# Kernel tuning notes

Measured on AMD Instinct MI355X. Metric: run time of the kernel, lower is better.

Reference implementation:

```python
import jax, jax.numpy as jnp
import numpy as np

# ---- static config (mirrors Spectral2xDown.__init__) ----
B, C_IN, C_OUT = 2, 256, 256
H_HI, W_HI = 256, 512
H_LO, W_LO = 128, 256
LMAX = H_LO            # 128
MMAX = W_LO // 2 + 1   # 129
GROUPS = 32
EPS_GN = 1e-5


def _cc_nodes_weights(n):
    """Clenshaw-Curtis nodes x_j=cos(pi*j/(n-1)) and quadrature weights on [-1,1]
    (torch_harmonics 'equiangular' grid)."""
    N = n - 1
    tj = np.pi * np.arange(n) / N
    xj = np.cos(tj)
    ks = np.arange(1, N // 2 + 1)
    b = np.where(2 * ks == N, 1.0, 2.0)
    s = (b / (4.0 * ks**2 - 1.0))[None, :] * np.cos(2.0 * ks[None, :] * tj[:, None])
    w = (2.0 / N) * (1.0 - s.sum(axis=1))
    w[0] = w[-1] = (1.0 / N**2) if (N % 2) else (1.0 / (N**2 - 1.0))
    return xj, w


def _legpoly(mmax, lmax, x):
    """Orthonormal associated Legendre (-1)^m c_lm P_lm(x), shape [mmax,lmax,len(x)]
    (torch_harmonics _precompute_legpoly, norm='ortho', csphase=True)."""
    nmax = max(mmax, lmax)
    vdm = np.zeros((nmax, nmax, len(x)))
    vdm[0, 0] = 1.0 / np.sqrt(4.0 * np.pi)
    for l in range(1, nmax):
        vdm[l - 1, l] = np.sqrt(2 * l + 1) * x * vdm[l - 1, l - 1]
        vdm[l, l] = np.sqrt((2 * l + 1) * (1 + x) * (1 - x) / (2 * l)) * vdm[l - 1, l - 1]
    for l in range(2, nmax):
        for m in range(0, l - 1):
            vdm[m, l] = (x * np.sqrt((2 * l - 1) / (l - m) * (2 * l + 1) / (l + m)) * vdm[m, l - 1]
                         - np.sqrt((l + m - 1) / (l - m) * (2 * l + 1) / (2 * l - 3)
                                   * (l - m - 1) / (l + m)) * vdm[m, l - 2])
    vdm = vdm[:mmax, :lmax].copy()
    for m in range(1, mmax, 2):  # Condon-Shortley phase
        vdm[m] *= -1.0
    return vdm


def _precompute():
    ct_hi, w_hi = _cc_nodes_weights(H_HI)
    pct_hi = _legpoly(MMAX, LMAX, np.flip(np.arccos(ct_hi)) * 0 + np.cos(np.flip(np.arccos(ct_hi))))
    wmat_hi = pct_hi * w_hi[None, None, :]          # quadrature folded in: [M,L,K_hi]
    ct_lo, _ = _cc_nodes_weights(H_LO)
    pct_lo = _legpoly(MMAX, LMAX, np.cos(np.flip(np.arccos(ct_lo))))  # [M,L,K_lo]
    return wmat_hi.astype(np.float32), pct_lo.astype(np.float32)


def setup_inputs() -> dict:
    key = jax.random.key(0)
    k1, k2 = jax.random.split(key, 2)
    x = jax.random.normal(k1, (B, C_IN, H_HI, W_HI), jnp.float32)
    conv_w = jax.random.normal(k2, (C_OUT, C_IN), jnp.float32) / np.sqrt(C_IN)
    conv_b = jnp.zeros((C_OUT,), jnp.float32)
    gamma = jnp.ones((C_OUT,), jnp.float32)
    beta = jnp.zeros((C_OUT,), jnp.float32)
    wmat_hi, pct_lo = _precompute()
    return {"x": x, "conv_w": conv_w, "conv_b": conv_b, "gamma": gamma, "beta": beta,
            "wmat_hi": jnp.asarray(wmat_hi), "pct_lo": jnp.asarray(pct_lo)}


def reference(x, conv_w, conv_b, gamma, beta, wmat_hi, pct_lo):
    # --- forward real SHT on high-res grid (2*pi * rfft(norm='forward') + Legendre quadrature) ---
    X = (2.0 * jnp.pi / W_HI) * jnp.fft.rfft(x, axis=-1)     # [B,C,K_hi,W_HI//2+1]
    X = X[..., :MMAX]                                        # truncate to mmax
    flm_r = jnp.einsum('bckm,mlk->bclm', X.real, wmat_hi)    # [B,C,L,M]
    flm_i = jnp.einsum('bckm,mlk->bclm', X.imag, wmat_hi)
    # --- inverse real SHT on low-res grid ---
    g = (jnp.einsum('bclm,mlk->bckm', flm_r, pct_lo)
         + 1j * jnp.einsum('bclm,mlk->bckm', flm_i, pct_lo))  # [B,C,K_lo,M]
    y = jnp.fft.irfft(g, n=W_LO, axis=-1) * W_LO             # irfft norm='forward'
    # --- 1x1 conv -> GroupNorm(32) -> exact GELU ---
    h = jnp.einsum('bchw,oc->bohw', y, conv_w) + conv_b[None, :, None, None]
    hg = h.reshape(B, GROUPS, C_OUT // GROUPS, H_LO, W_LO)
    mu = hg.mean(axis=(2, 3, 4), keepdims=True)
    var = ((hg - mu) ** 2).mean(axis=(2, 3, 4), keepdims=True)
    hn = ((hg - mu) * jax.lax.rsqrt(var + EPS_GN)).reshape(B, C_OUT, H_LO, W_LO)
    out = hn * gamma[None, :, None, None] + beta[None, :, None, None]
    return jax.nn.gelu(out, approximate=False)
```

## Files before the change

### kernel.cpp

```cpp
#include <hip/hip_runtime.h>
#include <math.h>


#define ROWS_HI 131072
#define ROWS_LO 65536

#define B_FT    0LL
#define B_FIT   262144LL
#define B_WM    393216LL
#define B_PCT   8781824LL
#define B_WB    12976128LL
#define B_STATS 13107200LL
#define B_R1    13107712LL
#define B_R2    80216576LL

typedef __attribute__((ext_vector_type(8))) short bf16x8;
typedef __attribute__((ext_vector_type(8))) unsigned short ushort8;
typedef __attribute__((ext_vector_type(4))) unsigned short ushort4v;
typedef __attribute__((ext_vector_type(4))) float f32x4;

__device__ inline unsigned short f2bf(float f){
  unsigned int u = __float_as_uint(f);
  unsigned int r = u + 0x7FFFu + ((u >> 16) & 1u);
  return (unsigned short)(r >> 16);
}

__global__ __launch_bounds__(256) void k_tables(unsigned char* __restrict__ ws){
  unsigned short* FT  = (unsigned short*)(ws + B_FT);
  unsigned short* FIT = (unsigned short*)(ws + B_FIT);
  float* stats = (float*)(ws + B_STATS);
  int idx = blockIdx.x*256 + threadIdx.x;
  if (idx < 131072){
    int p = idx >> 9, w = idx & 511, m = p >> 1;
    int pr = (m*w) & 511;
    float ang = (float)pr * (float)(2.0*M_PI/512.0);
    float s, c; sincosf(ang, &s, &c);
    const float S = (float)(2.0*M_PI/512.0);
    FT[idx] = f2bf((p & 1) ? (-S*s) : (S*c));
  }
  int i2 = idx - 131072;
  if (i2 >= 0 && i2 < 65536){
    int w = i2 >> 8, p = i2 & 255, m = p >> 1;
    float eps = (m == 0) ? 1.f : 2.f;
    int pr = (m*w) & 255;
    float ang = (float)pr * (float)(2.0*M_PI/256.0);
    float s, c; sincosf(ang, &s, &c);
    FIT[i2] = f2bf((p & 1) ? (-eps*s) : (eps*c));
  }
  int i3 = idx - (131072 + 65536);
  if (i3 >= 0 && i3 < 128) stats[i3] = 0.f;
}

__global__ __launch_bounds__(256) void k_prep(const float* __restrict__ wmat,
                                              const float* __restrict__ pct,
                                              const float* __restrict__ Wc,
                                              unsigned char* __restrict__ ws){
  unsigned short* WM = (unsigned short*)(ws + B_WM);
  unsigned short* PT = (unsigned short*)(ws + B_PCT);
  unsigned short* WB = (unsigned short*)(ws + B_WB);
  int idx = blockIdx.x*256 + threadIdx.x;
  if (idx < 4194304){
    WM[idx] = f2bf(wmat[idx]);
  } else if (idx < 6291456){
    int j = idx - 4194304;
    int m = j >> 14, kp = (j >> 7) & 127, l = j & 127;
    PT[j] = f2bf(pct[m*16384 + l*128 + kp]);
  } else if (idx < 6356992){
    int j = idx - 6291456;
    WB[j] = f2bf(Wc[j]);
  }
}

template<int AMODE, int CMODE, bool BIAS, int MT, int NT, int SKIP, int WPE>
__global__ __launch_bounds__(256, WPE) void k_gemm(
    const float* __restrict__ Af,
    const unsigned short* __restrict__ Abf,
    const unsigned short* __restrict__ Bt,
    float* __restrict__ Cf,
    unsigned short* __restrict__ Cbf,
    const float* __restrict__ bias,
    int ldA, int ldB, int ldC, int ksteps,
    long long sA, long long sB, int bzsh, long long sC)
{
  constexpr int BM = MT*32;
  constexpr int BN = NT*32;
  __shared__ unsigned short As[BM][40];
  __shared__ unsigned short Bs[BN][40];
  const int tid = threadIdx.x;
  const int z = blockIdx.z;
  const int m = z >> 1;
  const long long offA = (long long)z * sA;
  const long long offB = (long long)(z >> bzsh) * sB;
  const long long offC = (long long)z * sC;
  const int row0 = blockIdx.x * BM;
  const int n0   = blockIdx.y * BN;
  const int lane = tid & 63;
  const int wv = tid >> 6;
  const int wm = wv >> 1, wn = wv & 1;
  const int fr = lane & 15, q = lane >> 4;

  f32x4 acc[MT][NT];
#pragma unroll
  for (int i=0;i<MT;++i)
#pragma unroll
    for (int j=0;j<NT;++j) acc[i][j] = (f32x4){0.f,0.f,0.f,0.f};

  int ks0 = (SKIP == 2) ? (m >> 5) : 0;
  for (int ks = ks0; ks < ksteps; ++ks){
    const int k0 = ks * 32;
    if (AMODE == 0){
      if (BM == 128){
        const int row = tid >> 1, half = tid & 1;
        const float* s = Af + offA + (long long)(row0 + row) * ldA + k0 + half*16;
        float vv[16];
        *(float4*)(vv+0)  = *(const float4*)(s+0);
        *(float4*)(vv+4)  = *(const float4*)(s+4);
        *(float4*)(vv+8)  = *(const float4*)(s+8);
        *(float4*)(vv+12) = *(const float4*)(s+12);
        ushort8 H0, H1;
#pragma unroll
        for (int j=0;j<8;++j){ H0[j] = f2bf(vv[j]); H1[j] = f2bf(vv[8+j]); }
        *(ushort8*)&As[row][half*16]   = H0;
        *(ushort8*)&As[row][half*16+8] = H1;
      } else {
        const int row = tid >> 2, qt = tid & 3;
        const float* s = Af + offA + (long long)(row0 + row) * ldA + k0 + qt*8;
        float vv[8];
        *(float4*)(vv+0) = *(const float4*)(s+0);
        *(float4*)(vv+4) = *(const float4*)(s+4);
        ushort8 H;
#pragma unroll
        for (int j=0;j<8;++j) H[j] = f2bf(vv[j]);
        *(ushort8*)&As[row][qt*8] = H;
      }
    } else if (BM == 256){
      const unsigned short* s = Abf + offA + (long long)(row0 + tid) * ldA + k0;
      *(ushort8*)&As[tid][0]  = *(const ushort8*)(s);
      *(ushort8*)&As[tid][8]  = *(const ushort8*)(s+8);
      *(ushort8*)&As[tid][16] = *(const ushort8*)(s+16);
      *(ushort8*)&As[tid][24] = *(const ushort8*)(s+24);
    } else if (BM == 128){
      const int row = tid >> 1, half = tid & 1;
      const unsigned short* s = Abf + offA + (long long)(row0 + row) * ldA + k0 + half*16;
      *(ushort8*)&As[row][half*16]   = *(const ushort8*)(s);
      *(ushort8*)&As[row][half*16+8] = *(const ushort8*)(s+8);
    } else {
      const int row = tid >> 2, qt = tid & 3;
      const unsigned short* s = Abf + offA + (long long)(row0 + row) * ldA + k0 + qt*8;
      *(ushort8*)&As[row][qt*8] = *(const ushort8*)(s);
    }
    if (BN == 256){
      const unsigned short* s = Bt + offB + (long long)(n0 + tid) * ldB + k0;
      *(ushort8*)&Bs[tid][0]  = *(const ushort8*)(s);
      *(ushort8*)&Bs[tid][8]  = *(const ushort8*)(s+8);
      *(ushort8*)&Bs[tid][16] = *(const ushort8*)(s+16);
      *(ushort8*)&Bs[tid][24] = *(const ushort8*)(s+24);
    } else if (BN == 128){
      const int row = tid >> 1, half = tid & 1;
      const unsigned short* s = Bt + offB + (long long)(n0 + row) * ldB + k0 + half*16;
      *(ushort8*)&Bs[row][half*16]   = *(const ushort8*)(s);
      *(ushort8*)&Bs[row][half*16+8] = *(const ushort8*)(s+8);
    } else {
      const int row = tid >> 2, qt = tid & 3;
      const unsigned short* s = Bt + offB + (long long)(n0 + row) * ldB + k0 + qt*8;
      *(ushort8*)&Bs[row][qt*8] = *(const ushort8*)(s);
    }
    __syncthreads();
    bf16x8 ah[MT];
#pragma unroll
    for (int mt=0;mt<MT;++mt)
      ah[mt] = *(const bf16x8*)&As[wm*(MT*16)+mt*16+fr][q*8];
#pragma unroll
    for (int nt=0;nt<NT;++nt){
      if (SKIP == 1 && (wn*(NT*16) + nt*16 + 16 <= m)) continue;
      bf16x8 bb = *(const bf16x8*)&Bs[wn*(NT*16)+nt*16+fr][q*8];
#pragma unroll
      for (int mt=0;mt<MT;++mt)
        acc[mt][nt] = __builtin_amdgcn_mfma_f32_16x16x32_bf16(ah[mt], bb, acc[mt][nt], 0,0,0);
    }
    __syncthreads();
  }

  if (CMODE == 0){
#pragma unroll
    for (int mt=0;mt<MT;++mt){
      int row = row0 + wm*(MT*16) + mt*16 + q*4;
      float bv0=0.f,bv1=0.f,bv2=0.f,bv3=0.f;
      if (BIAS){ bv0=bias[row]; bv1=bias[row+1]; bv2=bias[row+2]; bv3=bias[row+3]; }
#pragma unroll
      for (int nt=0;nt<NT;++nt){
        int col = n0 + wn*(NT*16) + nt*16 + fr;
        float* dst = Cf + offC + (long long)row * ldC + col;
        dst[0]                = acc[mt][nt][0] + bv0;
        dst[(long long)ldC]   = acc[mt][nt][1] + bv1;
        dst[(long long)ldC*2] = acc[mt][nt][2] + bv2;
        dst[(long long)ldC*3] = acc[mt][nt][3] + bv3;
      }
    }
  } else if (CMODE == 1){
#pragma unroll
    for (int nt=0;nt<NT;++nt){
      int colp = n0 + wn*(NT*16) + nt*16 + fr;
#pragma unroll
      for (int mt=0;mt<MT;++mt){
        int rowb = row0 + wm*(MT*16) + mt*16 + q*4;
        ushort4v h;
        h[0] = f2bf(acc[mt][nt][0]);
        h[1] = f2bf(acc[mt][nt][1]);
        h[2] = f2bf(acc[mt][nt][2]);
        h[3] = f2bf(acc[mt][nt][3]);
        *(ushort4v*)&Cbf[offC + (long long)colp * ldC + rowb] = h;
      }
    }
  } else {
#pragma unroll
    for (int mt=0;mt<MT;++mt){
      int row = row0 + wm*(MT*16) + mt*16 + q*4;
#pragma unroll
      for (int nt=0;nt<NT;++nt){
        int col = n0 + wn*(NT*16) + nt*16 + fr;
        unsigned short* dst = Cbf + offC + (long long)row * ldC + col;
        dst[0]      = f2bf(acc[mt][nt][0]);
        dst[ldC]    = f2bf(acc[mt][nt][1]);
        dst[ldC*2]  = f2bf(acc[mt][nt][2]);
        dst[ldC*3]  = f2bf(acc[mt][nt][3]);
      }
    }
  }
}

__global__ __launch_bounds__(256) void k_trb(const unsigned short* __restrict__ g,
                                             unsigned short* __restrict__ gT){
  __shared__ unsigned short t[64][68];
  const int r0 = blockIdx.x * 64;
  const int p0 = blockIdx.y * 64;
  const int tr = threadIdx.x & 15, tc = threadIdx.x >> 4;
#pragma unroll
  for (int i=0;i<4;++i){
    int pl = tc + i*16;
    ushort4v v = *(const ushort4v*)(g + (long long)(p0+pl)*ROWS_LO + r0 + tr*4);
    *(ushort4v*)&t[pl][tr*4] = v;
  }
  __syncthreads();
#pragma unroll
  for (int i=0;i<4;++i){
    int rl = tc + i*16;
    ushort4v w;
    w[0]=t[tr*4+0][rl]; w[1]=t[tr*4+1][rl]; w[2]=t[tr*4+2][rl]; w[3]=t[tr*4+3][rl];
    *(ushort4v*)(gT + (long long)(r0+rl)*256 + p0 + tr*4) = w;
  }
}

__global__ __launch_bounds__(256) void k_tr2(const float* __restrict__ y,
                                             unsigned short* __restrict__ yT){
  __shared__ float t[64][65];
  const int s0 = blockIdx.x * 64;
  const int c0 = blockIdx.y * 64;
  const int b  = blockIdx.z;
  const int tr = threadIdx.x & 15, tc = threadIdx.x >> 4;
#pragma unroll
  for (int i=0;i<4;++i){
    int cl = tc + i*16;
    float4 v = *(const float4*)(y + (long long)b*8388608 + (long long)(c0+cl)*32768 + s0 + tr*4);
    t[cl][tr*4+0]=v.x; t[cl][tr*4+1]=v.y; t[cl][tr*4+2]=v.z; t[cl][tr*4+3]=v.w;
  }
  __syncthreads();
#pragma unroll
  for (int i=0;i<4;++i){
    int sl = tc + i*16;
    ushort4v w;
    w[0]=f2bf(t[tr*4+0][sl]); w[1]=f2bf(t[tr*4+1][sl]);
    w[2]=f2bf(t[tr*4+2][sl]); w[3]=f2bf(t[tr*4+3][sl]);
    *(ushort4v*)(yT + (long long)b*8388608 + (long long)(s0+sl)*256 + c0 + tr*4) = w;
  }
}

__global__ __launch_bounds__(256) void k_stats(const float* __restrict__ h,
                                               float* __restrict__ stats){
  const int bg = blockIdx.y;
  const int j  = blockIdx.x;
  const int t  = threadIdx.x;
  const float* base = h + (long long)bg*262144 + j*8192;
  float s = 0.f, ss = 0.f;
#pragma unroll
  for (int i=0;i<8;++i){
    float4 v = *(const float4*)(base + i*1024 + t*4);
    s  += v.x + v.y + v.z + v.w;
    ss += v.x*v.x + v.y*v.y + v.z*v.z + v.w*v.w;
  }
#pragma unroll
  for (int off=32; off>0; off>>=1){
    s  += __shfl_down(s, off, 64);
    ss += __shfl_down(ss, off, 64);
  }
  __shared__ float red[8];
  int wid = t >> 6;
  if ((t & 63) == 0){ red[wid*2] = s; red[wid*2+1] = ss; }
  __syncthreads();
  if (t == 0){
    float S  = red[0]+red[2]+red[4]+red[6];
    float SS = red[1]+red[3]+red[5]+red[7];
    atomicAdd(&stats[bg*2+0], S);
    atomicAdd(&stats[bg*2+1], SS);
  }
}

__global__ __launch_bounds__(256) void k_norm(float* __restrict__ out,
                                              const float* __restrict__ stats,
                                              const float* __restrict__ gamma,
                                              const float* __restrict__ beta){
  long long idx4 = ((long long)blockIdx.x*256 + threadIdx.x)*4;
  int o = (int)((idx4 >> 15) & 255);
  int b = (int)(idx4 >> 23);
  int bg = b*32 + (o >> 3);
  const float inv_n = 1.0f/262144.0f;
  float mean = stats[bg*2+0] * inv_n;
  float var  = stats[bg*2+1] * inv_n - mean*mean;
  float sc = rsqrtf(var + 1e-5f);
  float ga = gamma[o], be = beta[o];
  float4 v = *(float4*)(out + idx4);
  float t0 = (v.x - mean)*sc*ga + be;
  float t1 = (v.y - mean)*sc*ga + be;
  float t2 = (v.z - mean)*sc*ga + be;
  float t3 = (v.w - mean)*sc*ga + be;
  const float ISQ2 = 0.70710678118654752f;
  v.x = 0.5f*t0*(1.0f + erff(t0*ISQ2));
  v.y = 0.5f*t1*(1.0f + erff(t1*ISQ2));
  v.z = 0.5f*t2*(1.0f + erff(t2*ISQ2));
  v.w = 0.5f*t3*(1.0f + erff(t3*ISQ2));
  *(float4*)(out + idx4) = v;
}

extern "C" void kernel_launch(void* const* d_in, const int* in_sizes, int n_in,
                              void* d_out, int out_size, void* d_ws, size_t ws_size,
                              hipStream_t stream){
  const float* x      = (const float*)d_in[0];
  const float* conv_w = (const float*)d_in[1];
  const float* conv_b = (const float*)d_in[2];
  const float* gamma  = (const float*)d_in[3];
  const float* beta   = (const float*)d_in[4];
  const float* wmat   = (const float*)d_in[5];
  const float* pct    = (const float*)d_in[6];
  unsigned char* ws = (unsigned char*)d_ws;

  unsigned short* FT   = (unsigned short*)(ws + B_FT);
  unsigned short* FIT  = (unsigned short*)(ws + B_FIT);
  unsigned short* WM   = (unsigned short*)(ws + B_WM);
  unsigned short* PT   = (unsigned short*)(ws + B_PCT);
  unsigned short* WB   = (unsigned short*)(ws + B_WB);
  float*          stats= (float*)(ws + B_STATS);
  unsigned short* Xbf  = (unsigned short*)(ws + B_R1);
  unsigned short* gb   = (unsigned short*)(ws + B_R1);
  float*          y    = (float*)(ws + B_R1);
  unsigned short* flmb = (unsigned short*)(ws + B_R2);
  unsigned short* gTb  = (unsigned short*)(ws + B_R2);
  unsigned short* yT   = (unsigned short*)(ws + B_R2);
  float* out = (float*)d_out;

  k_tables<<<769, 256, 0, stream>>>(ws);
  k_prep  <<<24832, 256, 0, stream>>>(wmat, pct, conv_w, ws);

  k_gemm<0,1,false,2,8,0,3><<<dim3(2048,1,1), 256, 0, stream>>>(
      x, nullptr, FT, nullptr, Xbf, nullptr, 512, 512, ROWS_HI, 16, 0, 0, 0, 0);
  k_gemm<1,2,false,4,4,1,1><<<dim3(4,1,256), 256, 0, stream>>>(
      nullptr, Xbf, WM, nullptr, flmb, nullptr, 256, 256, 128, 8,
      131072LL, 32768LL, 1, 65536LL);
  k_gemm<1,2,false,4,4,2,1><<<dim3(4,1,256), 256, 0, stream>>>(
      nullptr, flmb, PT, nullptr, gb, nullptr, 128, 128, 128, 4,
      65536LL, 16384LL, 1, 65536LL);
  k_trb<<<dim3(1024,4), 256, 0, stream>>>(gb, gTb);
  k_gemm<1,0,false,2,8,0,3><<<dim3(1024,1,1), 256, 0, stream>>>(
      nullptr, gTb, FIT, y, nullptr, nullptr, 256, 256, 256, 8, 0, 0, 0, 0);
  k_tr2<<<dim3(512,4,2), 256, 0, stream>>>(y, yT);
  k_gemm<1,0,true,8,2,0,3><<<dim3(1,512,2), 256, 0, stream>>>(
      nullptr, WB, yT, out, nullptr, conv_b, 256, 256, 32768, 8,
      0, 8388608LL, 0, 8388608LL);

  k_stats<<<dim3(32,64), 256, 0, stream>>>(out, stats);
  k_norm <<<16384, 256, 0, stream>>>(out, stats, gamma, beta);
}
```

Before: 690.7 us.

## Double-buffer shared-memory tiles in GEMM with register prefetch of next k-step

The GEMM kernel now keeps two LDS buffers for A and B tiles and loads the next k-step's global data into registers while the MFMA loop consumes the current buffer. The register data is written to the alternate buffer afterwards, so only one barrier per iteration is needed. The goal is to hide global memory latency behind the matrix math. In exchange it doubles LDS and raises register pressure, so the launch-bounds waves hint is adjusted (3→2 for most GEMMs, 1→2 for the batched ones). The AMODE 0 path drops its BM==128 branch, which is fine because the only launch using it has BM 64.

```diff
diff --git a/kernel.cpp b/kernel.cpp
--- a/kernel.cpp
+++ b/kernel.cpp
@@ -84,8 +84,8 @@
 {
   constexpr int BM = MT*32;
   constexpr int BN = NT*32;
-  __shared__ unsigned short As[BM][40];
-  __shared__ unsigned short Bs[BN][40];
+  __shared__ unsigned short As[2][BM][40];
+  __shared__ unsigned short Bs[2][BN][40];
   const int tid = threadIdx.x;
   const int z = blockIdx.z;
   const int m = z >> 1;
@@ -99,86 +99,117 @@
   const int wm = wv >> 1, wn = wv & 1;
   const int fr = lane & 15, q = lane >> 4;
 
-  f32x4 acc[MT][NT];
-#pragma unroll
-  for (int i=0;i<MT;++i)
-#pragma unroll
-    for (int j=0;j<NT;++j) acc[i][j] = (f32x4){0.f,0.f,0.f,0.f};
-
-  int ks0 = (SKIP == 2) ? (m >> 5) : 0;
-  for (int ks = ks0; ks < ksteps; ++ks){
+  float   av[8];
+  ushort8 ar0, ar1, ar2, ar3;
+  ushort8 br0, br1, br2, br3;
+
+  auto loadA = [&](int ks){
     const int k0 = ks * 32;
     if (AMODE == 0){
-      if (BM == 128){
-        const int row = tid >> 1, half = tid & 1;
-        const float* s = Af + offA + (long long)(row0 + row) * ldA + k0 + half*16;
-        float vv[16];
-        *(float4*)(vv+0)  = *(const float4*)(s+0);
-        *(float4*)(vv+4)  = *(const float4*)(s+4);
-        *(float4*)(vv+8)  = *(const float4*)(s+8);
-        *(float4*)(vv+12) = *(const float4*)(s+12);
-        ushort8 H0, H1;
-#pragma unroll
-        for (int j=0;j<8;++j){ H0[j] = f2bf(vv[j]); H1[j] = f2bf(vv[8+j]); }
-        *(ushort8*)&As[row][half*16]   = H0;
-        *(ushort8*)&As[row][half*16+8] = H1;
-      } else {
-        const int row = tid >> 2, qt = tid & 3;
-        const float* s = Af + offA + (long long)(row0 + row) * ldA + k0 + qt*8;
-        float vv[8];
-        *(float4*)(vv+0) = *(const float4*)(s+0);
-        *(float4*)(vv+4) = *(const float4*)(s+4);
-        ushort8 H;
-#pragma unroll
-        for (int j=0;j<8;++j) H[j] = f2bf(vv[j]);
-        *(ushort8*)&As[row][qt*8] = H;
-      }
+      const int row = tid >> 2, qt = tid & 3;
+      const float* s = Af + offA + (long long)(row0 + row) * ldA + k0 + qt*8;
+      *(float4*)(av+0) = *(const float4*)(s+0);
+      *(float4*)(av+4) = *(const float4*)(s+4);
     } else if (BM == 256){
       const unsigned short* s = Abf + offA + (long long)(row0 + tid) * ldA + k0;
-      *(ushort8*)&As[tid][0]  = *(const ushort8*)(s);
-      *(ushort8*)&As[tid][8]  = *(const ushort8*)(s+8);
-      *(ushort8*)&As[tid][16] = *(const ushort8*)(s+16);
-      *(ushort8*)&As[tid][24] = *(const ushort8*)(s+24);
+      ar0 = *(const ushort8*)(s);    ar1 = *(const ushort8*)(s+8);
+      ar2 = *(const ushort8*)(s+16); ar3 = *(const ushort8*)(s+24);
     } else if (BM == 128){
       const int row = tid >> 1, half = tid & 1;
       const unsigned short* s = Abf + offA + (long long)(row0 + row) * ldA + k0 + half*16;
-      *(ushort8*)&As[row][half*16]   = *(const ushort8*)(s);
-      *(ushort8*)&As[row][half*16+8] = *(const ushort8*)(s+8);
+      ar0 = *(const ushort8*)(s); ar1 = *(const ushort8*)(s+8);
     } else {
       const int row = tid >> 2, qt = tid & 3;
       const unsigned short* s = Abf + offA + (long long)(row0 + row) * ldA + k0 + qt*8;
-      *(ushort8*)&As[row][qt*8] = *(const ushort8*)(s);
-    }
+      ar0 = *(const ushort8*)(s);
+    }
+  };
+  auto writeA = [&](int buf){
+    if (AMODE == 0){
+      const int row = tid >> 2, qt = tid & 3;
+      ushort8 H;
+#pragma unroll
+      for (int j=0;j<8;++j) H[j] = f2bf(av[j]);
+      *(ushort8*)&As[buf][row][qt*8] = H;
+    } else if (BM == 256){
+      *(ushort8*)&As[buf][tid][0]  = ar0;
+      *(ushort8*)&As[buf][tid][8]  = ar1;
+      *(ushort8*)&As[buf][tid][16] = ar2;
+      *(ushort8*)&As[buf][tid][24] = ar3;
+    } else if (BM == 128){
+      const int row = tid >> 1, half = tid & 1;
+      *(ushort8*)&As[buf][row][half*16]   = ar0;
+      *(ushort8*)&As[buf][row][half*16+8] = ar1;
+    } else {
+      const int row = tid >> 2, qt = tid & 3;
+      *(ushort8*)&As[buf][row][qt*8] = ar0;
+    }
+  };
+  auto loadB = [&](int ks){
+    const int k0 = ks * 32;
     if (BN == 256){
       const unsigned short* s = Bt + offB + (long long)(n0 + tid) * ldB + k0;
-      *(ushort8*)&Bs[tid][0]  = *(const ushort8*)(s);
-      *(ushort8*)&Bs[tid][8]  = *(const ushort8*)(s+8);
-      *(ushort8*)&Bs[tid][16] = *(const ushort8*)(s+16);
-      *(ushort8*)&Bs[tid][24] = *(const ushort8*)(s+24);
+      br0 = *(const ushort8*)(s);    br1 = *(const ushort8*)(s+8);
+      br2 = *(const ushort8*)(s+16); br3 = *(const ushort8*)(s+24);
     } else if (BN == 128){
       const int row = tid >> 1, half = tid & 1;
       const unsigned short* s = Bt + offB + (long long)(n0 + row) * ldB + k0 + half*16;
-      *(ushort8*)&Bs[row][half*16]   = *(const ushort8*)(s);
-      *(ushort8*)&Bs[row][half*16+8] = *(const ushort8*)(s+8);
+      br0 = *(const ushort8*)(s); br1 = *(const ushort8*)(s+8);
     } else {
       const int row = tid >> 2, qt = tid & 3;
       const unsigned short* s = Bt + offB + (long long)(n0 + row) * ldB + k0 + qt*8;
-      *(ushort8*)&Bs[row][qt*8] = *(const ushort8*)(s);
-    }
-    __syncthreads();
+      br0 = *(const ushort8*)(s);
+    }
+  };
+  auto writeB = [&](int buf){
+    if (BN == 256){
+      *(ushort8*)&Bs[buf][tid][0]  = br0;
+      *(ushort8*)&Bs[buf][tid][8]  = br1;
+      *(ushort8*)&Bs[buf][tid][16] = br2;
+      *(ushort8*)&Bs[buf][tid][24] = br3;
+    } else if (BN == 128){
+      const int row = tid >> 1, half = tid & 1;
+      *(ushort8*)&Bs[buf][row][half*16]   = br0;
+      *(ushort8*)&Bs[buf][row][half*16+8] = br1;
+    } else {
+      const int row = tid >> 2, qt = tid & 3;
+      *(ushort8*)&Bs[buf][row][qt*8] = br0;
+    }
+  };
+
+  f32x4 acc[MT][NT];
+#pragma unroll
+  for (int i=0;i<MT;++i)
+#pragma unroll
+    for (int j=0;j<NT;++j) acc[i][j] = (f32x4){0.f,0.f,0.f,0.f};
+
+  const int ks0 = (SKIP == 2) ? (m >> 5) : 0;
+
+  loadA(ks0); loadB(ks0);
+  writeA(0);  writeB(0);
+  __syncthreads();
+
+  int cur = 0;
+  for (int ks = ks0; ks < ksteps; ++ks){
+    const bool more = (ks + 1 < ksteps);
+    if (more){ loadA(ks+1); loadB(ks+1); }
     bf16x8 ah[MT];
 #pragma unroll
     for (int mt=0;mt<MT;++mt)
-      ah[mt] = *(const bf16x8*)&As[wm*(MT*16)+mt*16+fr][q*8];
+      ah[mt] = *(const bf16x8*)&As[cur][wm*(MT*16)+mt*16+fr][q*8];
 #pragma unroll
     for (int nt=0;nt<NT;++nt){
       if (SKIP == 1 && (wn*(NT*16) + nt*16 + 16 <= m)) continue;
-      bf16x8 bb = *(const bf16x8*)&Bs[wn*(NT*16)+nt*16+fr][q*8];
+      bf16x8 bb = *(const bf16x8*)&Bs[cur][wn*(NT*16)+nt*16+fr][q*8];
 #pragma unroll
       for (int mt=0;mt<MT;++mt)
         acc[mt][nt] = __builtin_amdgcn_mfma_f32_16x16x32_bf16(ah[mt], bb, acc[mt][nt], 0,0,0);
     }
-    __syncthreads();
+    if (more){
+      writeA(cur^1); writeB(cur^1);
+      __syncthreads();
+      cur ^= 1;
+    }
   }
 
   if (CMODE == 0){
@@ -360,19 +391,19 @@
   k_tables<<<769, 256, 0, stream>>>(ws);
   k_prep  <<<24832, 256, 0, stream>>>(wmat, pct, conv_w, ws);
 
-  k_gemm<0,1,false,2,8,0,3><<<dim3(2048,1,1), 256, 0, stream>>>(
+  k_gemm<0,1,false,2,8,0,2><<<dim3(2048,1,1), 256, 0, stream>>>(
       x, nullptr, FT, nullptr, Xbf, nullptr, 512, 512, ROWS_HI, 16, 0, 0, 0, 0);
-  k_gemm<1,2,false,4,4,1,1><<<dim3(4,1,256), 256, 0, stream>>>(
+  k_gemm<1,2,false,4,4,1,2><<<dim3(4,1,256), 256, 0, stream>>>(
       nullptr, Xbf, WM, nullptr, flmb, nullptr, 256, 256, 128, 8,
       131072LL, 32768LL, 1, 65536LL);
-  k_gemm<1,2,false,4,4,2,1><<<dim3(4,1,256), 256, 0, stream>>>(
+  k_gemm<1,2,false,4,4,2,2><<<dim3(4,1,256), 256, 0, stream>>>(
       nullptr, flmb, PT, nullptr, gb, nullptr, 128, 128, 128, 4,
       65536LL, 16384LL, 1, 65536LL);
   k_trb<<<dim3(1024,4), 256, 0, stream>>>(gb, gTb);
-  k_gemm<1,0,false,2,8,0,3><<<dim3(1024,1,1), 256, 0, stream>>>(
+  k_gemm<1,0,false,2,8,0,2><<<dim3(1024,1,1), 256, 0, stream>>>(
       nullptr, gTb, FIT, y, nullptr, nullptr, 256, 256, 256, 8, 0, 0, 0, 0);
   k_tr2<<<dim3(512,4,2), 256, 0, stream>>>(y, yT);
-  k_gemm<1,0,true,8,2,0,3><<<dim3(1,512,2), 256, 0, stream>>>(
+  k_gemm<1,0,true,8,2,0,2><<<dim3(1,512,2), 256, 0, stream>>>(
       nullptr, WB, yT, out, nullptr, conv_b, 256, 256, 32768, 8,
       0, 8388608LL, 0, 8388608LL);
 
```

Result: faster. 635.0 us (-8.1%).
